# Kernel tuning notes

Hardware: AMD Instinct MI355X
Metric: run time of the kernel (lower is better)

The kernel has to match this reference:

```python
import jax, jax.numpy as jnp
import numpy as np

C = 64            # x_channel (d_model)
D = 2 * C         # d_inner (expand=2)
N = C // 2        # d_state
K = 4             # scan directions
R = -(-C // 16)   # dt_rank = ceil(d_model/16)
Bsz, H, W = 2, 48, 48
EPS = 1e-5


def setup_inputs() -> dict:
    key = jax.random.key(0)
    ks = jax.random.split(key, 8)
    g = lambda k, shp, s: jax.random.normal(k, shp, dtype=jnp.float32) * s
    return {
        "fufea1": g(ks[0], (Bsz, C, H, W), 1.0),
        "ln_g": jnp.ones((C,), jnp.float32),
        "ln_b": jnp.zeros((C,), jnp.float32),
        "in_proj_w": g(ks[1], (2 * D, C), C ** -0.5),
        "conv_w": g(ks[2], (D, 1, 3, 3), 1.0 / 3.0),   # depthwise 3x3
        "conv_b": g(ks[3], (D,), 0.02),
        "x_proj_w": g(ks[4], (K, R + 2 * N, D), D ** -0.5),
        "dt_w": g(ks[5], (K, D, R), R ** -0.5),
        "dt_b": g(ks[6], (K, D), 0.1),
        "A_logs": jnp.log(jnp.tile(jnp.arange(1, N + 1, dtype=jnp.float32), (K, D, 1))),  # S4D-real init
        "Ds": jnp.ones((K, D), jnp.float32),
        "out_ln_g": jnp.ones((D,), jnp.float32),
        "out_ln_b": jnp.zeros((D,), jnp.float32),
        "out_proj_w": g(ks[7], (C, D), D ** -0.5),
    }


def _layernorm(x, g, b):
    mu = x.mean(-1, keepdims=True)
    var = ((x - mu) ** 2).mean(-1, keepdims=True)
    return (x - mu) * jax.lax.rsqrt(var + EPS) * g + b


def reference(fufea1, ln_g, ln_b, in_proj_w, conv_w, conv_b, x_proj_w,
              dt_w, dt_b, A_logs, Ds, out_ln_g, out_ln_b, out_proj_w):
    B, Cc, Hh, Ww = fufea1.shape
    L = Hh * Ww
    # pre-LN (over channels, channels-last)
    xn = _layernorm(fufea1.transpose(0, 2, 3, 1), ln_g, ln_b)          # (B,H,W,C)
    # SS2D: in_proj -> split x,z
    xz = xn @ in_proj_w.T                                               # (B,H,W,2D)
    x, z = jnp.split(xz, 2, axis=-1)
    x = x.transpose(0, 3, 1, 2)                                         # (B,D,H,W)
    x = jax.lax.conv_general_dilated(x, conv_w, (1, 1), "SAME",
                                     feature_group_count=D,
                                     dimension_numbers=("NCHW", "OIHW", "NCHW"))
    x = jax.nn.silu(x + conv_b[None, :, None, None])
    # 4-direction sequences: row-major, col-major, and their reverses
    x_hw = x.reshape(B, D, L)
    x_wh = x.transpose(0, 1, 3, 2).reshape(B, D, L)
    xs = jnp.stack([x_hw, x_wh], axis=1)                                # (B,2,D,L)
    xs = jnp.concatenate([xs, jnp.flip(xs, axis=-1)], axis=1)           # (B,K,D,L)
    # per-direction projections of dt, B, C
    x_dbl = jnp.einsum("bkdl,kcd->bkcl", xs, x_proj_w)
    dts, Bs, Cs = jnp.split(x_dbl, [R, R + N], axis=2)                  # (B,K,R,L),(B,K,N,L),(B,K,N,L)
    dts = jnp.einsum("bkrl,kdr->bkdl", dts, dt_w)
    delta = jax.nn.softplus(dts + dt_b[None, :, :, None])               # (B,K,D,L)
    A = -jnp.exp(A_logs)                                                # (K,D,N)
    # selective scan over L; carry h: (B,K,D,N)
    u_l = xs.transpose(3, 0, 1, 2)                                      # (L,B,K,D)
    dt_l = delta.transpose(3, 0, 1, 2)
    B_l = Bs.transpose(3, 0, 1, 2)                                      # (L,B,K,N)
    C_l = Cs.transpose(3, 0, 1, 2)

    def step(h, inp):
        u_t, d_t, b_t, c_t = inp
        dA = jnp.exp(d_t[..., None] * A)                                # (B,K,D,N)
        h = dA * h + (d_t * u_t)[..., None] * b_t[:, :, None, :]
        y = jnp.einsum("bkdn,bkn->bkd", h, c_t)
        return h, y

    h0 = jnp.zeros((B, K, D, N), xs.dtype)
    _, ys = jax.lax.scan(step, h0, (u_l, dt_l, B_l, C_l))               # ys: (L,B,K,D)
    out_y = ys.transpose(1, 2, 3, 0) + Ds[None, :, :, None] * xs        # (B,K,D,L)
    # merge the 4 directions back to row-major hw order
    inv_y = jnp.flip(out_y[:, 2:4], axis=-1)                            # (B,2,D,L)
    wh = lambda t: t.reshape(B, D, Ww, Hh).transpose(0, 1, 3, 2).reshape(B, D, L)
    y = out_y[:, 0] + inv_y[:, 0] + wh(out_y[:, 1]) + wh(inv_y[:, 1])   # (B,D,L)
    y = y.transpose(0, 2, 1).reshape(B, Hh, Ww, D)
    y = _layernorm(y, out_ln_g, out_ln_b) * jax.nn.silu(z)
    out = (y @ out_proj_w.T).transpose(0, 3, 1, 2) + fufea1             # residual add
    return out
```

## Files before the change

kernel.cpp:

```cpp
#include <hip/hip_runtime.h>

#define Cc 64
#define Dd 128
#define Nn 32
#define Kk 4
#define Rr 4
#define Bb 2
#define Hh 48
#define Ww 48
#define Ll 2304
#define EPSf 1e-5f
#define LCc 144

#if __has_builtin(__builtin_amdgcn_exp2f)
#define EXP2F __builtin_amdgcn_exp2f
#else
#define EXP2F exp2f
#endif

__device__ __forceinline__ float wsum64(float v) {
  v += __shfl_xor(v, 32);
  v += __shfl_xor(v, 16);
  v += __shfl_xor(v, 8);
  v += __shfl_xor(v, 4);
  v += __shfl_xor(v, 2);
  v += __shfl_xor(v, 1);
  return v;
}

__device__ __forceinline__ float hmax32(float v) {
  v = fmaxf(v, __shfl_xor(v, 1));
  v = fmaxf(v, __shfl_xor(v, 2));
  v = fmaxf(v, __shfl_xor(v, 4));
  v = fmaxf(v, __shfl_xor(v, 8));
  v = fmaxf(v, __shfl_xor(v, 16));
  return v;
}

__global__ __launch_bounds__(256) void k1_ln_inproj(
    const float* __restrict__ x, const float* __restrict__ g,
    const float* __restrict__ bta, const float* __restrict__ Wp,
    float* __restrict__ xin, float* __restrict__ zb)
{
  __shared__ float xS[16][65];
  __shared__ float xnS[16][64];
  __shared__ float xaS[128][17];
  const int tid = threadIdx.x;
  const int wv = tid >> 6, lane = tid & 63;
  const int pbase = blockIdx.x * 16;
  const int b = pbase / Ll;
  const int lbase = pbase % Ll;
  {
    const int c = tid >> 2, li0 = (tid & 3) * 4;
    const float4 v4 = *(const float4*)&x[(b * Cc + c) * Ll + lbase + li0];
    xS[li0 + 0][c] = v4.x;
    xS[li0 + 1][c] = v4.y;
    xS[li0 + 2][c] = v4.z;
    xS[li0 + 3][c] = v4.w;
  }
  __syncthreads();
  const float gv = g[lane], bv = bta[lane];
  for (int pi = 0; pi < 4; ++pi) {
    const int p = wv * 4 + pi;
    const float v = xS[p][lane];
    const float mu = wsum64(v) * (1.0f / 64.0f);
    const float dv = v - mu;
    const float var = wsum64(dv * dv) * (1.0f / 64.0f);
    const float rs = rsqrtf(var + EPSf);
    xnS[p][lane] = dv * rs * gv + bv;
  }
  __syncthreads();
  float acc[4][4];
  #pragma unroll
  for (int pi = 0; pi < 4; ++pi)
    #pragma unroll
    for (int m = 0; m < 4; ++m) acc[pi][m] = 0.f;
  const float4* W4 = (const float4*)Wp;
  #pragma unroll 4
  for (int c4 = 0; c4 < 16; ++c4) {
    float4 xn4[4];
    #pragma unroll
    for (int pi = 0; pi < 4; ++pi)
      xn4[pi] = ((const float4*)xnS[wv * 4 + pi])[c4];
    #pragma unroll
    for (int m = 0; m < 4; ++m) {
      const float4 w4 = W4[(lane + 64 * m) * 16 + c4];
      #pragma unroll
      for (int pi = 0; pi < 4; ++pi)
        acc[pi][m] += xn4[pi].x * w4.x + xn4[pi].y * w4.y +
                      xn4[pi].z * w4.z + xn4[pi].w * w4.w;
    }
  }
  #pragma unroll
  for (int pi = 0; pi < 4; ++pi) {
    const int l = lbase + wv * 4 + pi;
    zb[(b * Ll + l) * Dd + lane]      = acc[pi][2];
    zb[(b * Ll + l) * Dd + lane + 64] = acc[pi][3];
    xaS[lane][wv * 4 + pi]      = acc[pi][0];
    xaS[lane + 64][wv * 4 + pi] = acc[pi][1];
  }
  __syncthreads();
  const int d = tid >> 1, off = (tid & 1) * 8;
  float* dst = &xin[(b * Dd + d) * Ll + lbase + off];
  #pragma unroll
  for (int i = 0; i < 8; ++i) dst[i] = xaS[d][off + i];
}

__global__ __launch_bounds__(512) void k3_proj(
    const float* __restrict__ xin, const float* __restrict__ cw,
    const float* __restrict__ cb, const float* __restrict__ xpw,
    const float* __restrict__ dtw, const float* __restrict__ dtb,
    float* __restrict__ xc, float2* __restrict__ dd2,
    float* __restrict__ BCm)
{
  __shared__ float xinS[128][30];
  __shared__ float xvS[8][132];
  __shared__ float dtsS[8][16];
  const int t = threadIdx.x;
  const int pb = blockIdx.x * 8;
  const int b = pb / Ll;
  const int lb = pb % Ll;
  const int h0 = lb / Ww, w0 = lb % Ww;
  for (int i = t; i < 3840; i += 512) {
    const int d = i / 30, j = i % 30;
    const int r = j / 10, c = j % 10;
    const int hh = h0 + r - 1, ww = w0 + c - 1;
    float v = 0.f;
    if (hh >= 0 && hh < Hh && ww >= 0 && ww < Ww)
      v = xin[(b * Dd + d) * Ll + hh * Ww + ww];
    xinS[d][j] = v;
  }
  __syncthreads();
  for (int i = t; i < 1024; i += 512) {
    const int pi = i >> 7, d = i & 127;
    float acc = cb[d];
    #pragma unroll
    for (int r = 0; r < 3; ++r)
      #pragma unroll
      for (int c = 0; c < 3; ++c)
        acc += xinS[d][r * 10 + pi + c] * cw[d * 9 + r * 3 + c];
    const float sig = 1.0f / (1.0f + __expf(-acc));
    xvS[pi][d] = acc * sig;
  }
  __syncthreads();
  if (t < 272) {
    const int k = t / 68, c = t % 68;
    const size_t bkL = (size_t)(b * Kk + k) * Ll;
    float acc[8];
    #pragma unroll
    for (int pi = 0; pi < 8; ++pi) acc[pi] = 0.f;
    const float4* w4p = (const float4*)(xpw + (k * 68 + c) * 128);
    for (int d4 = 0; d4 < 32; ++d4) {
      const float4 w4 = w4p[d4];
      #pragma unroll
      for (int pi = 0; pi < 8; ++pi) {
        const float4 x4 = ((const float4*)xvS[pi])[d4];
        acc[pi] += x4.x * w4.x + x4.y * w4.y + x4.z * w4.z + x4.w * w4.w;
      }
    }
    #pragma unroll
    for (int pi = 0; pi < 8; ++pi) {
      const int l0 = lb + pi;
      const int h = l0 / Ww, w = l0 % Ww;
      int lk;
      if      (k == 0) lk = l0;
      else if (k == 1) lk = w * Hh + h;
      else if (k == 2) lk = Ll - 1 - l0;
      else             lk = Ll - 1 - (w * Hh + h);
      if (c < Rr)
        dtsS[pi][k * 4 + c] = acc[pi];
      else if (c < Rr + Nn)
        BCm[((bkL + lk) * Nn + (c - Rr)) * 2]     = acc[pi];
      else
        BCm[((bkL + lk) * Nn + (c - Rr - Nn)) * 2 + 1] = acc[pi];
    }
  } else {
    for (int i = t - 272; i < 1024; i += 240) {
      const int d = i >> 3, pi = i & 7;
      xc[(b * Dd + d) * Ll + lb + pi] = xvS[pi][d];
    }
  }
  __syncthreads();
  {
    const int k = t >> 7, dd = t & 127;
    const float4 dw = *(const float4*)&dtw[(k * Dd + dd) * 4];
    const float biasv = dtb[k * Dd + dd];
    float2* drow = dd2 + ((size_t)((b * Kk + k) * Dd) + dd) * Ll;
    float2 buf[8];
    #pragma unroll
    for (int pi = 0; pi < 8; ++pi) {
      const float a = biasv
          + dtsS[pi][k * 4 + 0] * dw.x + dtsS[pi][k * 4 + 1] * dw.y
          + dtsS[pi][k * 4 + 2] * dw.z + dtsS[pi][k * 4 + 3] * dw.w;
      const float sp = (a > 20.f) ? a : log1pf(__expf(a));
      buf[pi] = make_float2(sp, sp * xvS[pi][dd]);
    }
    if (k == 0) {
      float4* f4 = (float4*)(drow + lb);
      #pragma unroll
      for (int j = 0; j < 4; ++j)
        f4[j] = make_float4(buf[2 * j].x, buf[2 * j].y, buf[2 * j + 1].x, buf[2 * j + 1].y);
    } else if (k == 2) {
      float4* f4 = (float4*)(drow + (Ll - 8 - lb));
      #pragma unroll
      for (int j = 0; j < 4; ++j)
        f4[j] = make_float4(buf[7 - 2 * j].x, buf[7 - 2 * j].y, buf[6 - 2 * j].x, buf[6 - 2 * j].y);
    } else {
      #pragma unroll
      for (int pi = 0; pi < 8; ++pi) {
        const int l0 = lb + pi;
        const int h = l0 / Ww, w = l0 % Ww;
        int lk = w * Hh + h;
        if (k == 3) lk = Ll - 1 - lk;
        drow[lk] = buf[pi];
      }
    }
  }
}

__global__ __launch_bounds__(512) void k4_scan(
    const float2* __restrict__ dd2, const float* __restrict__ BCm,
    const float* __restrict__ Alogs, float* __restrict__ ys)
{
  __shared__ float hendS[16][32];
  __shared__ float carryS[16][32];
  __shared__ float sumDS[16];
  __shared__ float cmaxS[16];
  __shared__ float pS[16][8][36];
  const int tid = threadIdx.x;
  const int s = tid >> 5, n = tid & 31;
  const int blk = blockIdx.x;
  const int bk = blk & 7;
  const int d = blk >> 3;
  const int b = bk >> 2, k = bk & 3;
  const float An = -__expf(Alogs[(k * Dd + d) * Nn + n]);
  const float AnE = An * 1.44269504f;
  const size_t bkL = (size_t)(b * Kk + k) * Ll;
  const float2* dP = dd2 + ((size_t)((b * Kk + k) * Dd) + d) * Ll;
  const float2* bcP = (const float2*)BCm + bkL * Nn + n;
  const int lbeg = s * LCc;
  float* yP = ys + ((size_t)((b * Kk + k) * Dd) + d) * Ll + lbeg;
  const int rrow = n & 7, qtr = n >> 3;

  float h = 0.f, sumD = 0.f, cmx = 0.f;
  {
    const float4* q4 = (const float4*)(dP + lbeg);
    const float2* bcl = bcP + (size_t)lbeg * Nn;
    float4 qa = q4[0], qb = q4[1];
    float2 bc0 = bcl[0], bc1 = bcl[Nn], bc2 = bcl[2 * Nn], bc3 = bcl[3 * Nn];
    for (int t8 = 0; t8 < LCc / 8; ++t8) {
      #pragma unroll
      for (int half = 0; half < 2; ++half) {
        q4 += 2; bcl += 4 * Nn;
        const float4 qa_n = q4[0], qb_n = q4[1];
        const float2 bc0n = bcl[0], bc1n = bcl[Nn], bc2n = bcl[2 * Nn], bc3n = bcl[3 * Nn];
        h = EXP2F(qa.x * AnE) * h + qa.y * bc0.x; pS[s][half * 4 + 0][n] = h * bc0.y;
        h = EXP2F(qa.z * AnE) * h + qa.w * bc1.x; pS[s][half * 4 + 1][n] = h * bc1.y;
        h = EXP2F(qb.x * AnE) * h + qb.y * bc2.x; pS[s][half * 4 + 2][n] = h * bc2.y;
        h = EXP2F(qb.z * AnE) * h + qb.w * bc3.x; pS[s][half * 4 + 3][n] = h * bc3.y;
        sumD += (qa.x + qa.z) + (qb.x + qb.z);
        cmx = fmaxf(cmx, fmaxf(fmaxf(fabsf(bc0.y), fabsf(bc1.y)),
                               fmaxf(fabsf(bc2.y), fabsf(bc3.y))));
        qa = qa_n; qb = qb_n; bc0 = bc0n; bc1 = bc1n; bc2 = bc2n; bc3 = bc3n;
      }
      const float4 a4 = *(const float4*)&pS[s][rrow][qtr * 8];
      const float4 d4v = *(const float4*)&pS[s][rrow][qtr * 8 + 4];
      float sum = ((a4.x + a4.y) + (a4.z + a4.w)) + ((d4v.x + d4v.y) + (d4v.z + d4v.w));
      sum += __shfl_xor(sum, 8);
      sum += __shfl_xor(sum, 16);
      if (n < 8) yP[t8 * 8 + n] = sum;
    }
  }
  hendS[s][n] = h;
  const float cmxAll = hmax32(cmx);
  if (n == 0) { sumDS[s] = sumD; cmaxS[s] = cmxAll; }
  __syncthreads();
  if (tid < 32) {
    float carry = 0.f;
    #pragma unroll
    for (int s2 = 0; s2 < 16; ++s2) {
      carryS[s2][tid] = carry;
      carry = EXP2F(AnE * sumDS[s2]) * carry + hendS[s2][tid];
    }
  }
  __syncthreads();
  const float carry = carryS[s][n];
  const float mc = hmax32(fabsf(carry));
  const float AmaxE = hmax32(AnE);
  const float Pstop = log2f(mc * cmaxS[s] * 3.2e6f) / (-AmaxE);
  {
    float hc = carry, P = 0.f;
    const float4* q4 = (const float4*)(dP + lbeg);
    const float2* cl = bcP + (size_t)lbeg * Nn;
    for (int t8 = 0; t8 < LCc / 8; ++t8) {
      if (!(P < Pstop)) break;
      #pragma unroll
      for (int half = 0; half < 2; ++half) {
        const float4 qa = q4[0], qb = q4[1];
        q4 += 2;
        hc *= EXP2F(qa.x * AnE); pS[s][half * 4 + 0][n] = hc * cl[0].y;
        hc *= EXP2F(qa.z * AnE); pS[s][half * 4 + 1][n] = hc * cl[Nn].y;
        hc *= EXP2F(qb.x * AnE); pS[s][half * 4 + 2][n] = hc * cl[2 * Nn].y;
        hc *= EXP2F(qb.z * AnE); pS[s][half * 4 + 3][n] = hc * cl[3 * Nn].y;
        P += (qa.x + qa.z) + (qb.x + qb.z);
        cl += 4 * Nn;
      }
      const float4 a4 = *(const float4*)&pS[s][rrow][qtr * 8];
      const float4 d4v = *(const float4*)&pS[s][rrow][qtr * 8 + 4];
      float sum = ((a4.x + a4.y) + (a4.z + a4.w)) + ((d4v.x + d4v.y) + (d4v.z + d4v.w));
      sum += __shfl_xor(sum, 8);
      sum += __shfl_xor(sum, 16);
      if (n < 8) yP[t8 * 8 + n] += sum;
    }
  }
}

__global__ __launch_bounds__(256) void k5_merge(
    const float* __restrict__ ys, const float* __restrict__ zb,
    const float* __restrict__ og, const float* __restrict__ ob,
    const float* __restrict__ Wo, const float* __restrict__ resid,
    const float* __restrict__ xc, const float* __restrict__ DsP,
    float* __restrict__ out)
{
  __shared__ float ysS[4][16][128];
  __shared__ float tS[16][128];
  __shared__ float oS[64][17];
  __shared__ float xcS[16][128];
  const int tid = threadIdx.x;
  const int wv = tid >> 6, lane = tid & 63;
  const int tb = blockIdx.x;
  const int b = tb / 144;
  const int ti = tb % 144;
  const int tr = ti / 12, tc = ti % 12;
  const int h0 = tr * 4, w0 = tc * 4;
  {
    const int dch = tid & 127, half = tid >> 7;
    #pragma unroll
    for (int ii = 0; ii < 2; ++ii) {
      const int i = half * 2 + ii;
      const int l0 = (h0 + i) * Ww + w0;
      float4 v;
      v = *(const float4*)&xc[(b * Dd + dch) * Ll + l0];
      xcS[i * 4 + 0][dch] = v.x; xcS[i * 4 + 1][dch] = v.y;
      xcS[i * 4 + 2][dch] = v.z; xcS[i * 4 + 3][dch] = v.w;
      v = *(const float4*)&ys[((size_t)(b * Kk + 0) * Dd + dch) * Ll + l0];
      ysS[0][i * 4 + 0][dch] = v.x; ysS[0][i * 4 + 1][dch] = v.y;
      ysS[0][i * 4 + 2][dch] = v.z; ysS[0][i * 4 + 3][dch] = v.w;
      const int r2 = Ll - 4 - (h0 + i) * Ww - w0;
      v = *(const float4*)&ys[((size_t)(b * Kk + 2) * Dd + dch) * Ll + r2];
      ysS[2][i * 4 + 3][dch] = v.x; ysS[2][i * 4 + 2][dch] = v.y;
      ysS[2][i * 4 + 1][dch] = v.z; ysS[2][i * 4 + 0][dch] = v.w;
    }
    #pragma unroll
    for (int jj = 0; jj < 2; ++jj) {
      const int j = half * 2 + jj;
      const int l1 = (w0 + j) * Hh + h0;
      float4 v = *(const float4*)&ys[((size_t)(b * Kk + 1) * Dd + dch) * Ll + l1];
      ysS[1][0 * 4 + j][dch] = v.x; ysS[1][1 * 4 + j][dch] = v.y;
      ysS[1][2 * 4 + j][dch] = v.z; ysS[1][3 * 4 + j][dch] = v.w;
      const int r3 = Ll - 4 - (w0 + j) * Hh - h0;
      v = *(const float4*)&ys[((size_t)(b * Kk + 3) * Dd + dch) * Ll + r3];
      ysS[3][3 * 4 + j][dch] = v.x; ysS[3][2 * 4 + j][dch] = v.y;
      ysS[3][1 * 4 + j][dch] = v.z; ysS[3][0 * 4 + j][dch] = v.w;
    }
  }
  float sDs[2];
  #pragma unroll
  for (int m = 0; m < 2; ++m) {
    const int dch = lane + 64 * m;
    sDs[m] = DsP[dch] + DsP[Dd + dch] + DsP[2 * Dd + dch] + DsP[3 * Dd + dch];
  }
  __syncthreads();
  for (int pi = 0; pi < 4; ++pi) {
    const int p = wv * 4 + pi;
    const int l0 = (h0 + (p >> 2)) * Ww + w0 + (p & 3);
    float tv[2];
    #pragma unroll
    for (int m = 0; m < 2; ++m) {
      const int dch = lane + 64 * m;
      tv[m] = ysS[0][p][dch] + ysS[1][p][dch] + ysS[2][p][dch] + ysS[3][p][dch]
            + sDs[m] * xcS[p][dch];
    }
    const float mu = wsum64(tv[0] + tv[1]) * (1.0f / 128.0f);
    const float q = wsum64((tv[0] - mu) * (tv[0] - mu) +
                           (tv[1] - mu) * (tv[1] - mu)) * (1.0f / 128.0f);
    const float rs = rsqrtf(q + EPSf);
    #pragma unroll
    for (int m = 0; m < 2; ++m) {
      const int dch = lane + 64 * m;
      const float zz = zb[(size_t)(b * Ll + l0) * Dd + dch];
      const float sig = 1.0f / (1.0f + __expf(-zz));
      tS[p][dch] = ((tv[m] - mu) * rs * og[dch] + ob[dch]) * (zz * sig);
    }
  }
  __syncthreads();
  float acc[4] = {0.f, 0.f, 0.f, 0.f};
  const float4* W4 = (const float4*)Wo;
  for (int d4 = 0; d4 < 32; ++d4) {
    const float4 w4 = W4[lane * 32 + d4];
    #pragma unroll
    for (int pi = 0; pi < 4; ++pi) {
      const float4 t4 = ((const float4*)tS[wv * 4 + pi])[d4];
      acc[pi] += t4.x * w4.x + t4.y * w4.y + t4.z * w4.z + t4.w * w4.w;
    }
  }
  #pragma unroll
  for (int pi = 0; pi < 4; ++pi) oS[lane][wv * 4 + pi] = acc[pi];
  __syncthreads();
  const int c = tid >> 2, q = tid & 3;
  const size_t obase = (size_t)(b * Cc + c) * Ll + (size_t)(h0 + q) * Ww + w0;
  const float4 r4 = *(const float4*)(resid + obase);
  float4 o4;
  o4.x = oS[c][q * 4 + 0] + r4.x;
  o4.y = oS[c][q * 4 + 1] + r4.y;
  o4.z = oS[c][q * 4 + 2] + r4.z;
  o4.w = oS[c][q * 4 + 3] + r4.w;
  *(float4*)(out + obase) = o4;
}

extern "C" void kernel_launch(void* const* d_in, const int* in_sizes, int n_in,
                              void* d_out, int out_size, void* d_ws, size_t ws_size,
                              hipStream_t stream)
{
  (void)in_sizes; (void)n_in; (void)out_size; (void)ws_size;
  const float* fufea1     = (const float*)d_in[0];
  const float* ln_g       = (const float*)d_in[1];
  const float* ln_b       = (const float*)d_in[2];
  const float* in_proj_w  = (const float*)d_in[3];
  const float* conv_w     = (const float*)d_in[4];
  const float* conv_b     = (const float*)d_in[5];
  const float* x_proj_w   = (const float*)d_in[6];
  const float* dt_w       = (const float*)d_in[7];
  const float* dt_b       = (const float*)d_in[8];
  const float* A_logs     = (const float*)d_in[9];
  const float* Ds         = (const float*)d_in[10];
  const float* out_ln_g   = (const float*)d_in[11];
  const float* out_ln_b   = (const float*)d_in[12];
  const float* out_proj_w = (const float*)d_in[13];

  float* ws = (float*)d_ws;
  float2* dd2 = (float2*)ws;
  float* BCm  = ws + 4718592;
  float* zb   = ws + 5898240;
  float* xc   = ws + 6488064;
  float* ysb  = ws + 7077888;
  float* xin  = ws + 7077888;

  k1_ln_inproj<<<288, 256, 0, stream>>>(fufea1, ln_g, ln_b, in_proj_w, xin, zb);
  k3_proj<<<576, 512, 0, stream>>>(xin, conv_w, conv_b, x_proj_w, dt_w, dt_b,
                                   xc, dd2, BCm);
  k4_scan<<<1024, 512, 0, stream>>>(dd2, BCm, A_logs, ysb);
  k5_merge<<<288, 256, 0, stream>>>(ysb, zb, out_ln_g, out_ln_b, out_proj_w, fufea1,
                                    xc, Ds, (float*)d_out);
}
```

Measured before the change: 224.2 us.

## Split interleaved B/C buffer into planar arrays and deepen scan prefetch

The interleaved B/C float2 buffer is replaced by two separate planar arrays. The carry-correction pass can then read only C values instead of pulling whole float2 pairs. The first scan pass also gets a two-deep register prefetch pipeline, so loads for step i+2 are issued while step i computes. This raises register use and changes how k3_proj writes B and C, which may affect occupancy.

Result: faster. 208.0 us (-7.2%).

```diff
diff --git a/kernel.cpp b/kernel.cpp
--- a/kernel.cpp
+++ b/kernel.cpp
@@ -111,7 +111,7 @@
     const float* __restrict__ cb, const float* __restrict__ xpw,
     const float* __restrict__ dtw, const float* __restrict__ dtb,
     float* __restrict__ xc, float2* __restrict__ dd2,
-    float* __restrict__ BCm)
+    float* __restrict__ Bm, float* __restrict__ Cm)
 {
   __shared__ float xinS[128][30];
   __shared__ float xvS[8][132];
@@ -167,12 +167,9 @@
       else if (k == 1) lk = w * Hh + h;
       else if (k == 2) lk = Ll - 1 - l0;
       else             lk = Ll - 1 - (w * Hh + h);
-      if (c < Rr)
-        dtsS[pi][k * 4 + c] = acc[pi];
-      else if (c < Rr + Nn)
-        BCm[((bkL + lk) * Nn + (c - Rr)) * 2]     = acc[pi];
-      else
-        BCm[((bkL + lk) * Nn + (c - Rr - Nn)) * 2 + 1] = acc[pi];
+      if (c < Rr)            dtsS[pi][k * 4 + c] = acc[pi];
+      else if (c < Rr + Nn)  Bm[(bkL + lk) * Nn + (c - Rr)] = acc[pi];
+      else                   Cm[(bkL + lk) * Nn + (c - Rr - Nn)] = acc[pi];
     }
   } else {
     for (int i = t - 272; i < 1024; i += 240) {
@@ -219,8 +216,9 @@
 }
 
 __global__ __launch_bounds__(512) void k4_scan(
-    const float2* __restrict__ dd2, const float* __restrict__ BCm,
-    const float* __restrict__ Alogs, float* __restrict__ ys)
+    const float2* __restrict__ dd2, const float* __restrict__ Bm,
+    const float* __restrict__ Cm, const float* __restrict__ Alogs,
+    float* __restrict__ ys)
 {
   __shared__ float hendS[16][32];
   __shared__ float carryS[16][32];
@@ -237,7 +235,8 @@
   const float AnE = An * 1.44269504f;
   const size_t bkL = (size_t)(b * Kk + k) * Ll;
   const float2* dP = dd2 + ((size_t)((b * Kk + k) * Dd) + d) * Ll;
-  const float2* bcP = (const float2*)BCm + bkL * Nn + n;
+  const float* bP = Bm + bkL * Nn + n;
+  const float* cP = Cm + bkL * Nn + n;
   const int lbeg = s * LCc;
   float* yP = ys + ((size_t)((b * Kk + k) * Dd) + d) * Ll + lbeg;
   const int rrow = n & 7, qtr = n >> 3;
@@ -245,23 +244,39 @@
   float h = 0.f, sumD = 0.f, cmx = 0.f;
   {
     const float4* q4 = (const float4*)(dP + lbeg);
-    const float2* bcl = bcP + (size_t)lbeg * Nn;
-    float4 qa = q4[0], qb = q4[1];
-    float2 bc0 = bcl[0], bc1 = bcl[Nn], bc2 = bcl[2 * Nn], bc3 = bcl[3 * Nn];
+    const float* bl = bP + (size_t)lbeg * Nn;
+    const float* cl = cP + (size_t)lbeg * Nn;
+    float4 qa[2], qb[2];
+    float bv[2][4], cv[2][4];
+    #pragma unroll
+    for (int i = 0; i < 2; ++i) {
+      qa[i] = q4[2 * i]; qb[i] = q4[2 * i + 1];
+      #pragma unroll
+      for (int j = 0; j < 4; ++j) {
+        bv[i][j] = bl[(4 * i + j) * Nn];
+        cv[i][j] = cl[(4 * i + j) * Nn];
+      }
+    }
+    q4 += 4; bl += 8 * Nn; cl += 8 * Nn;
     for (int t8 = 0; t8 < LCc / 8; ++t8) {
       #pragma unroll
       for (int half = 0; half < 2; ++half) {
-        q4 += 2; bcl += 4 * Nn;
-        const float4 qa_n = q4[0], qb_n = q4[1];
-        const float2 bc0n = bcl[0], bc1n = bcl[Nn], bc2n = bcl[2 * Nn], bc3n = bcl[3 * Nn];
-        h = EXP2F(qa.x * AnE) * h + qa.y * bc0.x; pS[s][half * 4 + 0][n] = h * bc0.y;
-        h = EXP2F(qa.z * AnE) * h + qa.w * bc1.x; pS[s][half * 4 + 1][n] = h * bc1.y;
-        h = EXP2F(qb.x * AnE) * h + qb.y * bc2.x; pS[s][half * 4 + 2][n] = h * bc2.y;
-        h = EXP2F(qb.z * AnE) * h + qb.w * bc3.x; pS[s][half * 4 + 3][n] = h * bc3.y;
-        sumD += (qa.x + qa.z) + (qb.x + qb.z);
-        cmx = fmaxf(cmx, fmaxf(fmaxf(fabsf(bc0.y), fabsf(bc1.y)),
-                               fmaxf(fabsf(bc2.y), fabsf(bc3.y))));
-        qa = qa_n; qb = qb_n; bc0 = bc0n; bc1 = bc1n; bc2 = bc2n; bc3 = bc3n;
+        const float4 a = qa[half], bq = qb[half];
+        const float B0 = bv[half][0], B1 = bv[half][1], B2 = bv[half][2], B3 = bv[half][3];
+        const float C0 = cv[half][0], C1 = cv[half][1], C2 = cv[half][2], C3 = cv[half][3];
+        qa[half] = q4[0]; qb[half] = q4[1];
+        bv[half][0] = bl[0]; bv[half][1] = bl[Nn];
+        bv[half][2] = bl[2 * Nn]; bv[half][3] = bl[3 * Nn];
+        cv[half][0] = cl[0]; cv[half][1] = cl[Nn];
+        cv[half][2] = cl[2 * Nn]; cv[half][3] = cl[3 * Nn];
+        q4 += 2; bl += 4 * Nn; cl += 4 * Nn;
+        h = EXP2F(a.x * AnE) * h + a.y * B0;  pS[s][half * 4 + 0][n] = h * C0;
+        h = EXP2F(a.z * AnE) * h + a.w * B1;  pS[s][half * 4 + 1][n] = h * C1;
+        h = EXP2F(bq.x * AnE) * h + bq.y * B2; pS[s][half * 4 + 2][n] = h * C2;
+        h = EXP2F(bq.z * AnE) * h + bq.w * B3; pS[s][half * 4 + 3][n] = h * C3;
+        sumD += (a.x + a.z) + (bq.x + bq.z);
+        cmx = fmaxf(cmx, fmaxf(fmaxf(fabsf(C0), fabsf(C1)),
+                               fmaxf(fabsf(C2), fabsf(C3))));
       }
       const float4 a4 = *(const float4*)&pS[s][rrow][qtr * 8];
       const float4 d4v = *(const float4*)&pS[s][rrow][qtr * 8 + 4];
@@ -291,17 +306,17 @@
   {
     float hc = carry, P = 0.f;
     const float4* q4 = (const float4*)(dP + lbeg);
-    const float2* cl = bcP + (size_t)lbeg * Nn;
+    const float* cl = cP + (size_t)lbeg * Nn;
     for (int t8 = 0; t8 < LCc / 8; ++t8) {
       if (!(P < Pstop)) break;
       #pragma unroll
       for (int half = 0; half < 2; ++half) {
         const float4 qa = q4[0], qb = q4[1];
         q4 += 2;
-        hc *= EXP2F(qa.x * AnE); pS[s][half * 4 + 0][n] = hc * cl[0].y;
-        hc *= EXP2F(qa.z * AnE); pS[s][half * 4 + 1][n] = hc * cl[Nn].y;
-        hc *= EXP2F(qb.x * AnE); pS[s][half * 4 + 2][n] = hc * cl[2 * Nn].y;
-        hc *= EXP2F(qb.z * AnE); pS[s][half * 4 + 3][n] = hc * cl[3 * Nn].y;
+        hc *= EXP2F(qa.x * AnE); pS[s][half * 4 + 0][n] = hc * cl[0];
+        hc *= EXP2F(qa.z * AnE); pS[s][half * 4 + 1][n] = hc * cl[Nn];
+        hc *= EXP2F(qb.x * AnE); pS[s][half * 4 + 2][n] = hc * cl[2 * Nn];
+        hc *= EXP2F(qb.z * AnE); pS[s][half * 4 + 3][n] = hc * cl[3 * Nn];
         P += (qa.x + qa.z) + (qb.x + qb.z);
         cl += 4 * Nn;
       }
@@ -440,7 +455,8 @@
 
   float* ws = (float*)d_ws;
   float2* dd2 = (float2*)ws;
-  float* BCm  = ws + 4718592;
+  float* Bm   = ws + 4718592;
+  float* Cm   = ws + 5308416;
   float* zb   = ws + 5898240;
   float* xc   = ws + 6488064;
   float* ysb  = ws + 7077888;
@@ -448,8 +464,8 @@
 
   k1_ln_inproj<<<288, 256, 0, stream>>>(fufea1, ln_g, ln_b, in_proj_w, xin, zb);
   k3_proj<<<576, 512, 0, stream>>>(xin, conv_w, conv_b, x_proj_w, dt_w, dt_b,
-                                   xc, dd2, BCm);
-  k4_scan<<<1024, 512, 0, stream>>>(dd2, BCm, A_logs, ysb);
+                                   xc, dd2, Bm, Cm);
+  k4_scan<<<1024, 512, 0, stream>>>(dd2, Bm, Cm, A_logs, ysb);
   k5_merge<<<288, 256, 0, stream>>>(ysb, zb, out_ln_g, out_ln_b, out_proj_w, fufea1,
                                     xc, Ds, (float*)d_out);
 }
```
